# Performance work log

Hardware: AMD Instinct MI355X
Metric: run time of the kernel (lower is better)

The kernel has to match this reference:

```python
import jax, jax.numpy as jnp
import numpy as np

N = 128 * 128          # hardcoded in the original forward: x.view(1, 1, 128*128)
SCORE_LIMIT = int(0.5 * N)   # int(score_limit * num_inputs) = 8192
K = 7                  # odd kernel_size, padding = K // 2 = 3


def setup_inputs() -> dict:
    key = jax.random.key(0)
    k1, k2 = jax.random.split(key)
    x = jax.random.normal(k1, (N,), dtype=jnp.float32)
    # Conv1d(1, 1, K, bias=False) weight, flattened to a length-K taps vector
    conv_w = jax.random.normal(k2, (K,), dtype=jnp.float32) * 0.1
    return {"x": x, "conv_w": conv_w}


def reference(x, conv_w):
    # torch Conv1d is cross-correlation with 'same' padding (K odd):
    # y[i] = sum_j w[j] * x[i + j - K//2]. jnp.convolve flips the kernel,
    # so pass conv_w reversed to get cross-correlation.
    y = jnp.convolve(x, conv_w[::-1], mode="same")
    attention_score = jax.nn.sigmoid(y)                     # [N]
    attention_index = jnp.argsort(attention_score)          # ascending, [N]
    keep = attention_index[:SCORE_LIMIT]                    # lowest-score indices kept (as in source)
    simple_score = attention_score[keep] + 1.0              # [SCORE_LIMIT]
    # zeros everywhere, scatter rescaled values at kept indices
    new_x = jnp.zeros_like(x).at[keep].set(x[keep] * simple_score)
    return new_x, attention_score
```

## Files before the change

### kernel.cpp

```cpp
#include <hip/hip_runtime.h>
#include <math.h>

#define N 16384
#define LIMIT 8192
#define NT 1024
#define EPT 16

__global__ __launch_bounds__(1024) void fused_kernel(const float* __restrict__ x,
                                                     const float* __restrict__ w,
                                                     float* __restrict__ out) {
    __shared__ unsigned int hist0[1024 * 8];
    __shared__ unsigned int tot[4096];
    __shared__ unsigned int partial[256];
    __shared__ unsigned long long prefix_sh;
    __shared__ unsigned int r_sh;

    const int tid = threadIdx.x;
    const int base = tid * EPT;

    float wv[7];
#pragma unroll
    for (int t = 0; t < 7; ++t) wv[t] = w[t];

    float win[EPT + 6];
    const float4* xv = (const float4*)(x + base);
#pragma unroll
    for (int q = 0; q < 4; ++q) {
        float4 v = xv[q];
        win[3 + 4*q + 0] = v.x; win[3 + 4*q + 1] = v.y;
        win[3 + 4*q + 2] = v.z; win[3 + 4*q + 3] = v.w;
    }
#pragma unroll
    for (int t = 0; t < 3; ++t) {
        int jl = base - 3 + t;
        win[t] = (jl >= 0) ? x[jl] : 0.f;
        int jr = base + EPT + t;
        win[EPT + 3 + t] = (jr < N) ? x[jr] : 0.f;
    }

    float s[EPT];
#pragma unroll
    for (int k = 0; k < EPT; ++k) {
        float acc = 0.f;
#pragma unroll
        for (int t = 0; t < 7; ++t)
            acc = __fadd_rn(acc, __fmul_rn(win[k + t], wv[t]));
        s[k] = 1.f / (1.f + expf(-acc));
    }

    float4* so = (float4*)(out + N + base);
#pragma unroll
    for (int q = 0; q < 4; ++q)
        so[q] = make_float4(s[4*q], s[4*q+1], s[4*q+2], s[4*q+3]);

#pragma unroll
    for (int q = 0; q < 8; ++q) hist0[tid + q * 1024] = 0u;
#pragma unroll
    for (int q = 0; q < 4; ++q) tot[tid + q * 1024] = 0u;
    if (tid == 0) { prefix_sh = 0ULL; r_sh = LIMIT - 1; }
    __syncthreads();

    auto scan_select = [&](int W, int width) {
        const unsigned int r = r_sh;
        if (tid < 256) {
            unsigned int p = 0;
            for (int q = 0; q < W / 4; ++q) {
                uint4 v = ((const uint4*)tot)[tid * (W / 4) + q];
                p += v.x + v.y + v.z + v.w;
            }
            partial[tid] = p;
        }
        __syncthreads();
        if (tid < 64) {
            unsigned int p0 = partial[4*tid+0], p1 = partial[4*tid+1],
                         p2 = partial[4*tid+2], p3 = partial[4*tid+3];
            const unsigned int g4 = p0 + p1 + p2 + p3;
            unsigned int incl = g4;
#pragma unroll
            for (int d = 1; d < 64; d <<= 1) {
                unsigned int up = __shfl_up(incl, d, 64);
                if (tid >= d) incl += up;
            }
            unsigned long long ball = __ballot(incl > r);
            int L = __ffsll((unsigned long long)ball) - 1;
            if (tid == L) {
                unsigned int cum = incl - g4;
                unsigned int pp[4] = {p0, p1, p2, p3};
                int grp = -1;
#pragma unroll
                for (int k2 = 0; k2 < 4; ++k2) {
                    if (grp < 0) {
                        if (cum + pp[k2] > r) grp = 4*L + k2;
                        else cum += pp[k2];
                    }
                }
                unsigned int c[16];
                for (int q = 0; q < W / 4; ++q) {
                    uint4 v = ((const uint4*)tot)[grp * (W / 4) + q];
                    c[4*q+0] = v.x; c[4*q+1] = v.y; c[4*q+2] = v.z; c[4*q+3] = v.w;
                }
                int b = -1;
#pragma unroll
                for (int k2 = 0; k2 < 16; ++k2) {
                    if (k2 < W && b < 0) {
                        if (cum + c[k2] > r) b = grp * W + k2;
                        else cum += c[k2];
                    }
                }
                r_sh = r - cum;
                prefix_sh = (prefix_sh << width) | (unsigned long long)b;
            }
        }
        __syncthreads();
    };

    const int slot = tid & 7;
#pragma unroll
    for (int k = 0; k < EPT; ++k) {
        unsigned long long key = ((unsigned long long)__float_as_uint(s[k]) << 14)
                                 | (unsigned int)(base + k);
        unsigned int bin = (unsigned int)(key >> 34);
        atomicAdd(&hist0[bin * 8 + slot], 1u);
    }
    __syncthreads();
    {
        uint4 a = ((const uint4*)hist0)[tid * 2];
        uint4 b = ((const uint4*)hist0)[tid * 2 + 1];
        tot[tid] = a.x + a.y + a.z + a.w + b.x + b.y + b.z + b.w;
    }
    __syncthreads();
    scan_select(4, 10);

    const int widths[3] = {12, 11, 11};
    const int shifts[3] = {22, 11, 0};
    const int nbins[3]  = {4096, 2048, 2048};
#pragma unroll
    for (int p = 0; p < 3; ++p) {
        const int width = widths[p], shift = shifts[p], B = nbins[p];
        for (int b = tid; b < B; b += 1024) tot[b] = 0u;
        __syncthreads();
        const unsigned long long prefix = prefix_sh;
#pragma unroll
        for (int k = 0; k < EPT; ++k) {
            unsigned long long key = ((unsigned long long)__float_as_uint(s[k]) << 14)
                                     | (unsigned int)(base + k);
            if ((key >> (shift + width)) == prefix)
                atomicAdd(&tot[(unsigned int)(key >> shift) & (unsigned int)(B - 1)], 1u);
        }
        __syncthreads();
        scan_select(B / 256, width);
    }
    const unsigned long long T = prefix_sh;

    float4* no = (float4*)(out + base);
#pragma unroll
    for (int q = 0; q < 4; ++q) {
        float4 v;
        float* vp = &v.x;
#pragma unroll
        for (int e = 0; e < 4; ++e) {
            int k = 4*q + e;
            unsigned long long key = ((unsigned long long)__float_as_uint(s[k]) << 14)
                                     | (unsigned int)(base + k);
            vp[e] = (key <= T) ? __fmul_rn(win[3 + k], __fadd_rn(s[k], 1.0f)) : 0.f;
        }
        no[q] = v;
    }
}

extern "C" void kernel_launch(void* const* d_in, const int* in_sizes, int n_in,
                              void* d_out, int out_size, void* d_ws, size_t ws_size,
                              hipStream_t stream) {
    const float* x = (const float*)d_in[0];
    const float* w = (const float*)d_in[1];
    float* out = (float*)d_out;
    fused_kernel<<<1, NT, 0, stream>>>(x, w, out);
}
```

Before: 69.52 us.

## Replicate radix select across 16 blocks and add small-bucket candidate fast path

Launches 16 redundant blocks that each run the full radix-select, and each block writes only its own 1/16 slice of the outputs. The first histogram pass is shrunk to 4 slots per bin. After the second pass, if the threshold bucket holds at most 64 elements, the kernel collects those candidates and ranks them with a wave shuffle instead of running two more histogram passes. This removes passes and barriers on the common path, at the cost of redundant compute across blocks and extra branch complexity.

```diff
diff --git a/kernel.cpp b/kernel.cpp
--- a/kernel.cpp
+++ b/kernel.cpp
@@ -4,18 +4,85 @@
 #define N 16384
 #define LIMIT 8192
 #define NT 1024
+#define G 16
 #define EPT 16
 
-__global__ __launch_bounds__(1024) void fused_kernel(const float* __restrict__ x,
-                                                     const float* __restrict__ w,
-                                                     float* __restrict__ out) {
-    __shared__ unsigned int hist0[1024 * 8];
-    __shared__ unsigned int tot[4096];
-    __shared__ unsigned int partial[256];
+
+__device__ __forceinline__ unsigned long long make_key(float s, int i) {
+    return ((unsigned long long)__float_as_uint(s) << 14) | (unsigned int)i;
+}
+
+template <int W, int WIDTH>
+__device__ __forceinline__ void scan_select(unsigned int* tot,
+                                            unsigned int* partial,
+                                            unsigned long long* prefix_sh,
+                                            unsigned int* r_sh,
+                                            unsigned int* m_sh) {
+    const int tid = threadIdx.x;
+    const unsigned int r = *r_sh;
+    if (tid < 256) {
+        unsigned int p = 0;
+#pragma unroll
+        for (int q = 0; q < W / 4; ++q) {
+            uint4 v = ((const uint4*)tot)[tid * (W / 4) + q];
+            p += v.x + v.y + v.z + v.w;
+        }
+        partial[tid] = p;
+    }
+    __syncthreads();
+    if (tid < 64) {
+        unsigned int p0 = partial[4*tid+0], p1 = partial[4*tid+1],
+                     p2 = partial[4*tid+2], p3 = partial[4*tid+3];
+        const unsigned int g4 = p0 + p1 + p2 + p3;
+        unsigned int incl = g4;
+#pragma unroll
+        for (int d = 1; d < 64; d <<= 1) {
+            unsigned int up = __shfl_up(incl, d, 64);
+            if (tid >= d) incl += up;
+        }
+        unsigned long long ball = __ballot(incl > r);
+        int L = __ffsll((long long)ball) - 1;
+        if (tid == L) {
+            unsigned int cum = incl - g4;
+            unsigned int pp[4] = {p0, p1, p2, p3};
+            int grp = -1;
+#pragma unroll
+            for (int k = 0; k < 4; ++k)
+                if (grp < 0) { if (cum + pp[k] > r) grp = 4*L + k; else cum += pp[k]; }
+            unsigned int c[W];
+#pragma unroll
+            for (int q = 0; q < W / 4; ++q) {
+                uint4 v = ((const uint4*)tot)[grp * (W / 4) + q];
+                c[4*q+0] = v.x; c[4*q+1] = v.y; c[4*q+2] = v.z; c[4*q+3] = v.w;
+            }
+            int b = -1; unsigned int mm = 0;
+#pragma unroll
+            for (int k = 0; k < W; ++k)
+                if (b < 0) {
+                    if (cum + c[k] > r) { b = grp * W + k; mm = c[k]; }
+                    else cum += c[k];
+                }
+            *r_sh = r - cum;
+            *m_sh = mm;
+            *prefix_sh = (*prefix_sh << WIDTH) | (unsigned long long)b;
+        }
+    }
+    __syncthreads();
+}
+
+__global__ __launch_bounds__(NT)
+void mono_kernel(const float* __restrict__ x, const float* __restrict__ w,
+                 float* __restrict__ out) {
+    __shared__ __attribute__((aligned(16))) unsigned int hist0[4096];
+    __shared__ __attribute__((aligned(16))) unsigned int tot[1024];
+    __shared__ __attribute__((aligned(16))) unsigned int hist1[4096];
+    __shared__ __attribute__((aligned(16))) unsigned int partial[256];
     __shared__ unsigned long long prefix_sh;
-    __shared__ unsigned int r_sh;
+    __shared__ unsigned int r_sh, m_sh, ccnt, tlow_sh;
+    __shared__ unsigned int cand[64];
 
     const int tid = threadIdx.x;
+    const int blk = blockIdx.x;
     const int base = tid * EPT;
 
     float wv[7];
@@ -38,6 +105,11 @@
         win[EPT + 3 + t] = (jr < N) ? x[jr] : 0.f;
     }
 
+    hist0[tid] = 0; hist0[tid+1024] = 0; hist0[tid+2048] = 0; hist0[tid+3072] = 0;
+    hist1[tid] = 0; hist1[tid+1024] = 0; hist1[tid+2048] = 0; hist1[tid+3072] = 0;
+    tot[tid] = 0;
+    if (tid == 0) { prefix_sh = 0ULL; r_sh = LIMIT - 1; ccnt = 0; }
+
     float s[EPT];
 #pragma unroll
     for (int k = 0; k < EPT; ++k) {
@@ -48,123 +120,109 @@
         s[k] = 1.f / (1.f + expf(-acc));
     }
 
-    float4* so = (float4*)(out + N + base);
-#pragma unroll
-    for (int q = 0; q < 4; ++q)
-        so[q] = make_float4(s[4*q], s[4*q+1], s[4*q+2], s[4*q+3]);
-
-#pragma unroll
-    for (int q = 0; q < 8; ++q) hist0[tid + q * 1024] = 0u;
-#pragma unroll
-    for (int q = 0; q < 4; ++q) tot[tid + q * 1024] = 0u;
-    if (tid == 0) { prefix_sh = 0ULL; r_sh = LIMIT - 1; }
-    __syncthreads();
-
-    auto scan_select = [&](int W, int width) {
-        const unsigned int r = r_sh;
-        if (tid < 256) {
-            unsigned int p = 0;
-            for (int q = 0; q < W / 4; ++q) {
-                uint4 v = ((const uint4*)tot)[tid * (W / 4) + q];
-                p += v.x + v.y + v.z + v.w;
-            }
-            partial[tid] = p;
+    if ((tid >> 6) == blk) {
+        float4* so = (float4*)(out + N + base);
+#pragma unroll
+        for (int q = 0; q < 4; ++q)
+            so[q] = make_float4(s[4*q], s[4*q+1], s[4*q+2], s[4*q+3]);
+    }
+    __syncthreads();
+
+    const int slot = tid & 3;
+#pragma unroll
+    for (int k = 0; k < EPT; ++k) {
+        unsigned int bin = __float_as_uint(s[k]) >> 20;
+        atomicAdd(&hist0[(bin << 2) | slot], 1u);
+    }
+    __syncthreads();
+    {
+        uint4 v = ((const uint4*)hist0)[tid];
+        tot[tid] = v.x + v.y + v.z + v.w;
+    }
+    __syncthreads();
+    scan_select<4, 10>(tot, partial, &prefix_sh, &r_sh, &m_sh);
+
+    {
+        const unsigned long long pref = prefix_sh;
+#pragma unroll
+        for (int k = 0; k < EPT; ++k) {
+            unsigned long long key = make_key(s[k], base + k);
+            if ((key >> 34) == pref)
+                atomicAdd(&hist1[(unsigned int)(key >> 22) & 4095u], 1u);
+        }
+    }
+    __syncthreads();
+    scan_select<16, 12>(hist1, partial, &prefix_sh, &r_sh, &m_sh);
+
+    unsigned long long T;
+    const unsigned int M = m_sh;
+    const unsigned int r1 = r_sh;
+    if (M <= 64u) {
+        const unsigned long long pref = prefix_sh;
+#pragma unroll
+        for (int k = 0; k < EPT; ++k) {
+            unsigned long long key = make_key(s[k], base + k);
+            if ((key >> 22) == pref) {
+                unsigned int pos = atomicAdd(&ccnt, 1u);
+                cand[pos] = (unsigned int)(key & 0x3FFFFFu);
+            }
         }
         __syncthreads();
         if (tid < 64) {
-            unsigned int p0 = partial[4*tid+0], p1 = partial[4*tid+1],
-                         p2 = partial[4*tid+2], p3 = partial[4*tid+3];
-            const unsigned int g4 = p0 + p1 + p2 + p3;
-            unsigned int incl = g4;
-#pragma unroll
-            for (int d = 1; d < 64; d <<= 1) {
-                unsigned int up = __shfl_up(incl, d, 64);
-                if (tid >= d) incl += up;
-            }
-            unsigned long long ball = __ballot(incl > r);
-            int L = __ffsll((unsigned long long)ball) - 1;
-            if (tid == L) {
-                unsigned int cum = incl - g4;
-                unsigned int pp[4] = {p0, p1, p2, p3};
-                int grp = -1;
-#pragma unroll
-                for (int k2 = 0; k2 < 4; ++k2) {
-                    if (grp < 0) {
-                        if (cum + pp[k2] > r) grp = 4*L + k2;
-                        else cum += pp[k2];
-                    }
-                }
-                unsigned int c[16];
-                for (int q = 0; q < W / 4; ++q) {
-                    uint4 v = ((const uint4*)tot)[grp * (W / 4) + q];
-                    c[4*q+0] = v.x; c[4*q+1] = v.y; c[4*q+2] = v.z; c[4*q+3] = v.w;
-                }
-                int b = -1;
-#pragma unroll
-                for (int k2 = 0; k2 < 16; ++k2) {
-                    if (k2 < W && b < 0) {
-                        if (cum + c[k2] > r) b = grp * W + k2;
-                        else cum += c[k2];
-                    }
-                }
-                r_sh = r - cum;
-                prefix_sh = (prefix_sh << width) | (unsigned long long)b;
-            }
-        }
-        __syncthreads();
-    };
-
-    const int slot = tid & 7;
-#pragma unroll
-    for (int k = 0; k < EPT; ++k) {
-        unsigned long long key = ((unsigned long long)__float_as_uint(s[k]) << 14)
-                                 | (unsigned int)(base + k);
-        unsigned int bin = (unsigned int)(key >> 34);
-        atomicAdd(&hist0[bin * 8 + slot], 1u);
-    }
-    __syncthreads();
-    {
-        uint4 a = ((const uint4*)hist0)[tid * 2];
-        uint4 b = ((const uint4*)hist0)[tid * 2 + 1];
-        tot[tid] = a.x + a.y + a.z + a.w + b.x + b.y + b.z + b.w;
-    }
-    __syncthreads();
-    scan_select(4, 10);
-
-    const int widths[3] = {12, 11, 11};
-    const int shifts[3] = {22, 11, 0};
-    const int nbins[3]  = {4096, 2048, 2048};
-#pragma unroll
-    for (int p = 0; p < 3; ++p) {
-        const int width = widths[p], shift = shifts[p], B = nbins[p];
-        for (int b = tid; b < B; b += 1024) tot[b] = 0u;
-        __syncthreads();
-        const unsigned long long prefix = prefix_sh;
-#pragma unroll
-        for (int k = 0; k < EPT; ++k) {
-            unsigned long long key = ((unsigned long long)__float_as_uint(s[k]) << 14)
-                                     | (unsigned int)(base + k);
-            if ((key >> (shift + width)) == prefix)
-                atomicAdd(&tot[(unsigned int)(key >> shift) & (unsigned int)(B - 1)], 1u);
-        }
-        __syncthreads();
-        scan_select(B / 256, width);
-    }
-    const unsigned long long T = prefix_sh;
-
-    float4* no = (float4*)(out + base);
-#pragma unroll
-    for (int q = 0; q < 4; ++q) {
-        float4 v;
-        float* vp = &v.x;
-#pragma unroll
-        for (int e = 0; e < 4; ++e) {
-            int k = 4*q + e;
-            unsigned long long key = ((unsigned long long)__float_as_uint(s[k]) << 14)
-                                     | (unsigned int)(base + k);
-            vp[e] = (key <= T) ? __fmul_rn(win[3 + k], __fadd_rn(s[k], 1.0f)) : 0.f;
-        }
-        no[q] = v;
+            unsigned int v = (tid < (int)M) ? cand[tid] : 0xFFFFFFFFu;
+            unsigned int cnt = 0;
+#pragma unroll
+            for (int i = 0; i < 64; ++i) {
+                unsigned int vi = __shfl(v, i, 64);
+                cnt += (vi < v) ? 1u : 0u;
+            }
+            if (tid < (int)M && cnt == r1) tlow_sh = v;
+        }
+        __syncthreads();
+        T = (prefix_sh << 22) | (unsigned long long)tlow_sh;
+    } else {
+        hist1[tid] = 0; hist1[tid + 1024] = 0;
+        __syncthreads();
+        {
+            const unsigned long long pref = prefix_sh;
+#pragma unroll
+            for (int k = 0; k < EPT; ++k) {
+                unsigned long long key = make_key(s[k], base + k);
+                if ((key >> 22) == pref)
+                    atomicAdd(&hist1[(unsigned int)(key >> 11) & 2047u], 1u);
+            }
+        }
+        __syncthreads();
+        scan_select<8, 11>(hist1, partial, &prefix_sh, &r_sh, &m_sh);
+        hist1[tid] = 0; hist1[tid + 1024] = 0;
+        __syncthreads();
+        {
+            const unsigned long long pref = prefix_sh;
+#pragma unroll
+            for (int k = 0; k < EPT; ++k) {
+                unsigned long long key = make_key(s[k], base + k);
+                if ((key >> 11) == pref)
+                    atomicAdd(&hist1[(unsigned int)key & 2047u], 1u);
+            }
+        }
+        __syncthreads();
+        scan_select<8, 11>(hist1, partial, &prefix_sh, &r_sh, &m_sh);
+        T = prefix_sh;
+    }
+
+    if ((tid >> 6) == blk) {
+        float4* no = (float4*)(out + base);
+#pragma unroll
+        for (int q = 0; q < 4; ++q) {
+            float4 v; float* vp = &v.x;
+#pragma unroll
+            for (int e = 0; e < 4; ++e) {
+                int k = 4*q + e;
+                unsigned long long key = make_key(s[k], base + k);
+                vp[e] = (key <= T) ? __fmul_rn(win[3 + k], __fadd_rn(s[k], 1.0f)) : 0.f;
+            }
+            no[q] = v;
+        }
     }
 }
 
@@ -174,5 +232,5 @@
     const float* x = (const float*)d_in[0];
     const float* w = (const float*)d_in[1];
     float* out = (float*)d_out;
-    fused_kernel<<<1, NT, 0, stream>>>(x, w, out);
-}
+    mono_kernel<<<G, NT, 0, stream>>>(x, w, out);
+}
```

Measured after the change: 65.50 us. -5.8%, faster.
